# Optimization experiments

Measured on AMD Instinct MI355X. Metric: run time of the kernel, lower is better.

The kernel has to match this reference:

```python
import jax, jax.numpy as jnp
import numpy as np


def setup_inputs() -> dict:
    key = jax.random.key(0)
    k1, k2 = jax.random.split(key)
    B, C, H, W, K = 4, 3, 384, 384, 15
    data = jax.random.normal(k1, (B, C, H, W), dtype=jnp.float32)
    kernels = jax.random.normal(k2, (B, K, K, H, W), dtype=jnp.float32)
    return {"data": data, "kernels": kernels}


def reference(data, kernels):
    # data: [B, 3, H, W]; kernels: [B, K, K, H, W] (per-pixel spatially-varying filter)
    B, C, H, W = data.shape
    K = kernels.shape[1]
    p = K // 2
    # flip both kernel dims then flatten taps: [B, K*K, H, W]
    kf = jnp.flip(kernels, axis=(1, 2)).reshape(B, K * K, H, W)
    data_pad = jnp.pad(data, ((0, 0), (0, 0), (p, p), (p, p)))

    def body(acc, q):
        i = q // K
        j = q % K
        # shifted window of the padded image: [B, C, H, W]
        patch = jax.lax.dynamic_slice(data_pad, (0, 0, i, j), (B, C, H, W))
        acc = acc + kf[:, q][:, None, :, :] * patch
        return acc, None

    acc0 = jnp.zeros((B, C, H, W), dtype=data.dtype)
    pred, _ = jax.lax.scan(body, acc0, jnp.arange(K * K))
    return pred
```

## Files before the change

kernel.cpp:

```cpp
#include <hip/hip_runtime.h>

#define BB 4
#define CC 3
#define HH 384
#define WW 384
#define KK 15
#define PP 7
#define HP (HH + 2*PP)
#define WP 400
#define HW (HH*WW)

#define TX 128
#define TY 8
#define SROWS (TY + 2*PP)
#define SCOLS (TX + 16)
#define NTX (WW / TX)
#define NTY (HH / TY)

__global__ __launch_bounds__(256) void pad_kernel(const float* __restrict__ data,
                                                  float* __restrict__ pad) {
    int idx = blockIdx.x * 256 + threadIdx.x;
    const int total = BB * CC * HP * WP;
    if (idx >= total) return;
    int x  = idx % WP;
    int y  = (idx / WP) % HP;
    int bc = idx / (WP * HP);
    int dy = y - PP, dx = x - PP;
    float v = 0.f;
    if (dy >= 0 && dy < HH && dx >= 0 && dx < WW)
        v = data[(size_t)bc * HW + dy * WW + dx];
    pad[idx] = v;
}

__global__ __launch_bounds__(256) void conv_tiled(const float* __restrict__ kern,
                                                  const float* __restrict__ pad,
                                                  float* __restrict__ out) {
    const int tid = threadIdx.x;
    const int blk = blockIdx.x;
    const int b   = blk / (NTY * NTX);
    const int r2  = blk - b * (NTY * NTX);
    const int ty  = r2 / NTX;
    const int tx  = r2 - ty * NTX;
    const int x0  = tx * TX;
    const int y0  = ty * TY;

    __shared__ __align__(16) float smem[CC][SROWS][SCOLS];

    const int NV = CC * SROWS * (SCOLS / 4);
    for (int i = tid; i < NV; i += 256) {
        int cx = i % (SCOLS / 4);
        int r  = (i / (SCOLS / 4)) % SROWS;
        int c  = i / ((SCOLS / 4) * SROWS);
        float4 d = *(const float4*)(pad + ((size_t)(b * CC + c) * HP + y0 + r) * WP
                                        + x0 + cx * 4);
        *(float4*)&smem[c][r][cx * 4] = d;
    }
    __syncthreads();

    const int lx = tid & 31;
    const int ly = tid >> 5;
    const int x  = x0 + lx * 4;
    const int y  = y0 + ly;
    const int pix = y * WW + x;

    const float* kb = kern + (size_t)b * (KK * KK) * HW + pix;

    float acc[CC][4];
    #pragma unroll
    for (int c = 0; c < CC; ++c)
        #pragma unroll
        for (int k = 0; k < 4; ++k) acc[c][k] = 0.f;

    #pragma unroll 1
    for (int u = 0; u < KK; ++u) {
        float4 kv[KK];
        #pragma unroll
        for (int v = 0; v < KK; ++v)
            kv[v] = *(const float4*)(kb + (size_t)(u * KK + v) * HW);

        const int rr = ly + 2 * PP - u;

        #pragma unroll
        for (int c = 0; c < CC; ++c) {
            float win[20];
            #pragma unroll
            for (int w = 0; w < 5; ++w) {
                float4 d = *(const float4*)&smem[c][rr][lx * 4 + w * 4];
                win[w * 4 + 0] = d.x;
                win[w * 4 + 1] = d.y;
                win[w * 4 + 2] = d.z;
                win[w * 4 + 3] = d.w;
            }
            #pragma unroll
            for (int v = 0; v < KK; ++v) {
                const int s = (KK - 1) - v;
                const float* kvp = (const float*)&kv[v];
                #pragma unroll
                for (int k = 0; k < 4; ++k)
                    acc[c][k] = fmaf(kvp[k], win[s + k], acc[c][k]);
            }
        }
    }

    #pragma unroll
    for (int c = 0; c < CC; ++c) {
        float4 o = make_float4(acc[c][0], acc[c][1], acc[c][2], acc[c][3]);
        *(float4*)(out + (size_t)(b * CC + c) * HW + pix) = o;
    }
}

__global__ __launch_bounds__(256) void conv_kernel_safe(const float* __restrict__ kern,
                                                        const float* __restrict__ data,
                                                        float* __restrict__ out) {
    const int t     = blockIdx.x * 256 + threadIdx.x;
    const int per_b = HW / 4;
    const int b   = t / per_b;
    const int r   = t - b * per_b;
    const int pix = r * 4;
    const int y   = pix / WW;
    const int x   = pix - y * WW;

    const float* kb = kern + (size_t)b * (KK * KK) * HW + pix;

    float acc[CC][4];
    #pragma unroll
    for (int c = 0; c < CC; ++c)
        #pragma unroll
        for (int k = 0; k < 4; ++k) acc[c][k] = 0.f;

    #pragma unroll 1
    for (int u = 0; u < KK; ++u) {
        float4 kv[KK];
        #pragma unroll
        for (int v = 0; v < KK; ++v)
            kv[v] = *(const float4*)(kb + (size_t)(u * KK + v) * HW);

        const int drow  = y + PP - u;
        const bool rowok = (drow >= 0) && (drow < HH);

        #pragma unroll
        for (int c = 0; c < CC; ++c) {
            const float* dr = data + (size_t)(b * CC + c) * HW + drow * WW;
            float win[20];
            #pragma unroll
            for (int i = 0; i < 20; ++i) {
                int col = x + i - PP;
                win[i] = (rowok && col >= 0 && col < WW) ? dr[col] : 0.f;
            }
            #pragma unroll
            for (int v = 0; v < KK; ++v) {
                const int s = (KK - 1) - v;
                const float* kvp = (const float*)&kv[v];
                #pragma unroll
                for (int k = 0; k < 4; ++k)
                    acc[c][k] = fmaf(kvp[k], win[s + k], acc[c][k]);
            }
        }
    }

    #pragma unroll
    for (int c = 0; c < CC; ++c) {
        float4 o = make_float4(acc[c][0], acc[c][1], acc[c][2], acc[c][3]);
        *(float4*)(out + (size_t)(b * CC + c) * HW + pix) = o;
    }
}

extern "C" void kernel_launch(void* const* d_in, const int* in_sizes, int n_in,
                              void* d_out, int out_size, void* d_ws, size_t ws_size,
                              hipStream_t stream) {
    const float* data = (const float*)d_in[0];
    const float* kern = (const float*)d_in[1];
    float* out = (float*)d_out;

    const size_t padBytes = (size_t)BB * CC * HP * WP * sizeof(float);

    if (ws_size >= padBytes) {
        float* pad = (float*)d_ws;
        const int totalPad = BB * CC * HP * WP;
        pad_kernel<<<(totalPad + 255) / 256, 256, 0, stream>>>(data, pad);
        const int nBlocks = BB * NTY * NTX;
        conv_tiled<<<nBlocks, 256, 0, stream>>>(kern, pad, out);
    } else {
        const int nThreads = BB * HW / 4;
        conv_kernel_safe<<<nThreads / 256, 256, 0, stream>>>(kern, data, out);
    }
}
```

Before: 112.0 us.

## Fuse zero-padding into tiled conv load and use nontemporal kernel loads

```diff
diff --git a/kernel.cpp b/kernel.cpp
--- a/kernel.cpp
+++ b/kernel.cpp
@@ -1,4 +1,6 @@
 #include <hip/hip_runtime.h>
+
+typedef float f32x4 __attribute__((ext_vector_type(4)));
 
 #define BB 4
 #define CC 3
@@ -6,35 +8,20 @@
 #define WW 384
 #define KK 15
 #define PP 7
-#define HP (HH + 2*PP)
-#define WP 400
 #define HW (HH*WW)
 
 #define TX 128
-#define TY 8
-#define SROWS (TY + 2*PP)
-#define SCOLS (TX + 16)
+#define TY 6
 #define NTX (WW / TX)
 #define NTY (HH / TY)
+#define SROWS (TY + 2*PP)
+#define SCOLS 144
+#define SV (SCOLS / 4)
+#define NTHREADS 192
 
-__global__ __launch_bounds__(256) void pad_kernel(const float* __restrict__ data,
-                                                  float* __restrict__ pad) {
-    int idx = blockIdx.x * 256 + threadIdx.x;
-    const int total = BB * CC * HP * WP;
-    if (idx >= total) return;
-    int x  = idx % WP;
-    int y  = (idx / WP) % HP;
-    int bc = idx / (WP * HP);
-    int dy = y - PP, dx = x - PP;
-    float v = 0.f;
-    if (dy >= 0 && dy < HH && dx >= 0 && dx < WW)
-        v = data[(size_t)bc * HW + dy * WW + dx];
-    pad[idx] = v;
-}
-
-__global__ __launch_bounds__(256) void conv_tiled(const float* __restrict__ kern,
-                                                  const float* __restrict__ pad,
-                                                  float* __restrict__ out) {
+__global__ __launch_bounds__(NTHREADS) void conv_fused(const float* __restrict__ kern,
+                                                       const float* __restrict__ data,
+                                                       float* __restrict__ out) {
     const int tid = threadIdx.x;
     const int blk = blockIdx.x;
     const int b   = blk / (NTY * NTX);
@@ -46,14 +33,17 @@
 
     __shared__ __align__(16) float smem[CC][SROWS][SCOLS];
 
-    const int NV = CC * SROWS * (SCOLS / 4);
-    for (int i = tid; i < NV; i += 256) {
-        int cx = i % (SCOLS / 4);
-        int r  = (i / (SCOLS / 4)) % SROWS;
-        int c  = i / ((SCOLS / 4) * SROWS);
-        float4 d = *(const float4*)(pad + ((size_t)(b * CC + c) * HP + y0 + r) * WP
-                                        + x0 + cx * 4);
-        *(float4*)&smem[c][r][cx * 4] = d;
+    const int NV = CC * SROWS * SV;
+    for (int i = tid; i < NV; i += NTHREADS) {
+        int cx = i % SV;
+        int r  = (i / SV) % SROWS;
+        int c  = i / (SV * SROWS);
+        int drow = y0 + r - PP;
+        int dcol = x0 - 8 + cx * 4;
+        f32x4 v = {0.f, 0.f, 0.f, 0.f};
+        if (drow >= 0 && drow < HH && dcol >= 0 && dcol <= WW - 4)
+            v = *(const f32x4*)(data + ((size_t)(b * CC + c) * HH + drow) * WW + dcol);
+        *(f32x4*)&smem[c][r][cx * 4] = v;
     }
     __syncthreads();
 
@@ -73,10 +63,11 @@
 
     #pragma unroll 1
     for (int u = 0; u < KK; ++u) {
-        float4 kv[KK];
+        f32x4 kv[KK];
         #pragma unroll
         for (int v = 0; v < KK; ++v)
-            kv[v] = *(const float4*)(kb + (size_t)(u * KK + v) * HW);
+            kv[v] = __builtin_nontemporal_load(
+                        (const f32x4*)(kb + (size_t)(u * KK + v) * HW));
 
         const int rr = ly + 2 * PP - u;
 
@@ -85,7 +76,7 @@
             float win[20];
             #pragma unroll
             for (int w = 0; w < 5; ++w) {
-                float4 d = *(const float4*)&smem[c][rr][lx * 4 + w * 4];
+                f32x4 d = *(const f32x4*)&smem[c][rr][lx * 4 + w * 4];
                 win[w * 4 + 0] = d.x;
                 win[w * 4 + 1] = d.y;
                 win[w * 4 + 2] = d.z;
@@ -93,7 +84,7 @@
             }
             #pragma unroll
             for (int v = 0; v < KK; ++v) {
-                const int s = (KK - 1) - v;
+                const int s = KK - v;
                 const float* kvp = (const float*)&kv[v];
                 #pragma unroll
                 for (int k = 0; k < 4; ++k)
@@ -104,64 +95,8 @@
 
     #pragma unroll
     for (int c = 0; c < CC; ++c) {
-        float4 o = make_float4(acc[c][0], acc[c][1], acc[c][2], acc[c][3]);
-        *(float4*)(out + (size_t)(b * CC + c) * HW + pix) = o;
-    }
-}
-
-__global__ __launch_bounds__(256) void conv_kernel_safe(const float* __restrict__ kern,
-                                                        const float* __restrict__ data,
-                                                        float* __restrict__ out) {
-    const int t     = blockIdx.x * 256 + threadIdx.x;
-    const int per_b = HW / 4;
-    const int b   = t / per_b;
-    const int r   = t - b * per_b;
-    const int pix = r * 4;
-    const int y   = pix / WW;
-    const int x   = pix - y * WW;
-
-    const float* kb = kern + (size_t)b * (KK * KK) * HW + pix;
-
-    float acc[CC][4];
-    #pragma unroll
-    for (int c = 0; c < CC; ++c)
-        #pragma unroll
-        for (int k = 0; k < 4; ++k) acc[c][k] = 0.f;
-
-    #pragma unroll 1
-    for (int u = 0; u < KK; ++u) {
-        float4 kv[KK];
-        #pragma unroll
-        for (int v = 0; v < KK; ++v)
-            kv[v] = *(const float4*)(kb + (size_t)(u * KK + v) * HW);
-
-        const int drow  = y + PP - u;
-        const bool rowok = (drow >= 0) && (drow < HH);
-
-        #pragma unroll
-        for (int c = 0; c < CC; ++c) {
-            const float* dr = data + (size_t)(b * CC + c) * HW + drow * WW;
-            float win[20];
-            #pragma unroll
-            for (int i = 0; i < 20; ++i) {
-                int col = x + i - PP;
-                win[i] = (rowok && col >= 0 && col < WW) ? dr[col] : 0.f;
-            }
-            #pragma unroll
-            for (int v = 0; v < KK; ++v) {
-                const int s = (KK - 1) - v;
-                const float* kvp = (const float*)&kv[v];
-                #pragma unroll
-                for (int k = 0; k < 4; ++k)
-                    acc[c][k] = fmaf(kvp[k], win[s + k], acc[c][k]);
-            }
-        }
-    }
-
-    #pragma unroll
-    for (int c = 0; c < CC; ++c) {
-        float4 o = make_float4(acc[c][0], acc[c][1], acc[c][2], acc[c][3]);
-        *(float4*)(out + (size_t)(b * CC + c) * HW + pix) = o;
+        f32x4 o = {acc[c][0], acc[c][1], acc[c][2], acc[c][3]};
+        __builtin_nontemporal_store(o, (f32x4*)(out + (size_t)(b * CC + c) * HW + pix));
     }
 }
 
@@ -172,16 +107,6 @@
     const float* kern = (const float*)d_in[1];
     float* out = (float*)d_out;
 
-    const size_t padBytes = (size_t)BB * CC * HP * WP * sizeof(float);
-
-    if (ws_size >= padBytes) {
-        float* pad = (float*)d_ws;
-        const int totalPad = BB * CC * HP * WP;
-        pad_kernel<<<(totalPad + 255) / 256, 256, 0, stream>>>(data, pad);
-        const int nBlocks = BB * NTY * NTX;
-        conv_tiled<<<nBlocks, 256, 0, stream>>>(kern, pad, out);
-    } else {
-        const int nThreads = BB * HW / 4;
-        conv_kernel_safe<<<nThreads / 256, 256, 0, stream>>>(kern, data, out);
-    }
+    const int nBlocks = BB * NTY * NTX;
+    conv_fused<<<nBlocks, NTHREADS, 0, stream>>>(kern, data, out);
 }
```

New measurement: 92.91 us. -17.0%, faster.
